# Kernel optimization log

Hardware: AMD Instinct MI355X
Metric: run time of the kernel (lower is better)

## Reference

```python
import jax, jax.numpy as jnp
import numpy as np


def setup_inputs() -> dict:
    key = jax.random.key(0)
    k1, k2 = jax.random.split(key)
    B, N, M = 8, 8192, 8192
    input1 = jax.random.normal(k1, (B, N, 3), dtype=jnp.float32)
    input2 = jax.random.normal(k2, (B, M, 3), dtype=jnp.float32)
    return {"input1": input1, "input2": input2}


def _chamfer(xyz1, xyz2):
    # xyz1: [B, N, 3], xyz2: [B, M, 3]
    sq1 = jnp.sum(xyz1 * xyz1, axis=-1)              # [B, N]
    sq2 = jnp.sum(xyz2 * xyz2, axis=-1)              # [B, M]
    cross = jnp.einsum("bnd,bmd->bnm", xyz1, xyz2)  # [B, N, M]
    d = sq1[:, :, None] + sq2[:, None, :] - 2.0 * cross
    dist1 = jnp.min(d, axis=2)  # [B, N] nearest in xyz2 for each pt of xyz1
    dist2 = jnp.min(d, axis=1)  # [B, M]
    return dist1, dist2


def reference(input1, input2):
    return _chamfer(input1, input2)
```

## Files before the change

kernel.cpp:

```cpp
#include <hip/hip_runtime.h>


typedef __attribute__((ext_vector_type(8))) short  s16x8;
typedef __attribute__((ext_vector_type(16))) float f32x16;
typedef unsigned int u32;

#define TSLICE 512
#define QPB    512
#define QPW    128

__device__ inline u32 umin3(u32 a, u32 b, u32 c) {
    const u32 t = a < b ? a : b;
    return t < c ? t : c;
}

__device__ inline void mfma_fold_phys(const s16x8 a, const s16x8 b, u32& best) {
    asm volatile(
        "v_mfma_f32_32x32x16_bf16 v[40:55], %1, %2, 0\n\t"
        "s_nop 7\n\t"
        "s_nop 7\n\t"
        "s_nop 7\n\t"
        "v_min3_u32 v56, v40, v41, v42\n\t"
        "v_min3_u32 v57, v43, v44, v45\n\t"
        "v_min3_u32 v58, v46, v47, v48\n\t"
        "v_min3_u32 v59, v49, v50, v51\n\t"
        "v_min3_u32 v60, v52, v53, v54\n\t"
        "v_min3_u32 v56, v56, v57, v55\n\t"
        "v_min3_u32 v58, v58, v59, v60\n\t"
        "v_min3_u32 %0, v56, v58, %0"
        : "+v"(best)
        : "v"(a), "v"(b)
        : "v40","v41","v42","v43","v44","v45","v46","v47",
          "v48","v49","v50","v51","v52","v53","v54","v55",
          "v56","v57","v58","v59","v60");
}

__device__ inline unsigned int bf16bits(float v, float &hival) {
    unsigned int u = __float_as_uint(v);
    unsigned int r = (u + 0x7FFFu + ((u >> 16) & 1u)) >> 16;
    hival = __uint_as_float(r << 16);
    return r;
}

__global__ __launch_bounds__(256)
void pack_all_kernel(const float* __restrict__ in1, const float* __restrict__ in2,
                     ushort* __restrict__ A1, ushort* __restrict__ B1, float* __restrict__ S1,
                     ushort* __restrict__ A2, ushort* __restrict__ B2, float* __restrict__ S2,
                     unsigned int* __restrict__ out, int P1, int P2) {
    const int g = blockIdx.x * 256 + threadIdx.x;
    if (g >= P1 + P2) return;
    out[g] = 0x7F7F7F7Fu;

    const float* src; ushort* pA; ushort* pB; float* sq; int p;
    if (g < P1) { src = in1; pA = A1; pB = B1; sq = S1; p = g; }
    else        { src = in2; pA = A2; pB = B2; sq = S2; p = g - P1; }

    const float x = src[3*p+0], y = src[3*p+1], z = src[3*p+2];
    float xhf, xlf, yhf, ylf, zhf, zlf, shf, tmp;
    const ushort xh = (ushort)bf16bits(x, xhf);
    const ushort xl = (ushort)bf16bits(x - xhf, xlf);
    const ushort yh = (ushort)bf16bits(y, yhf);
    const ushort yl = (ushort)bf16bits(y - yhf, ylf);
    const ushort zh = (ushort)bf16bits(z, zhf);
    const ushort zl = (ushort)bf16bits(z - zhf, zlf);
    const float s = fmaf(x, x, fmaf(y, y, z * z));
    const ushort sh = (ushort)bf16bits(s, shf);
    const ushort sl = (ushort)bf16bits(s - shf, tmp);
    const ushort m2xh = (ushort)bf16bits(-2.0f * xhf, tmp);
    const ushort m2xl = (ushort)bf16bits(-2.0f * xlf, tmp);
    const ushort m2yh = (ushort)bf16bits(-2.0f * yhf, tmp);
    const ushort m2yl = (ushort)bf16bits(-2.0f * ylf, tmp);
    const ushort m2zh = (ushort)bf16bits(-2.0f * zhf, tmp);
    const ushort m2zl = (ushort)bf16bits(-2.0f * zlf, tmp);
    const ushort ONE  = 0x3F80;
    const ushort BIAS = 0x4400;

    const s16x8 a0 = {(short)m2xh,(short)m2xl,(short)m2xh,(short)m2xl,
                      (short)m2yh,(short)m2yl,(short)m2yh,(short)m2yl};
    const s16x8 a1 = {(short)m2zh,(short)m2zl,(short)m2zh,(short)m2zl,
                      (short)sh,  (short)sl,  (short)BIAS, 0};
    const s16x8 b0 = {(short)xh,(short)xh,(short)xl,(short)xl,
                      (short)yh,(short)yh,(short)yl,(short)yl};
    const s16x8 b1 = {(short)zh,(short)zh,(short)zl,(short)zl,
                      (short)ONE,(short)ONE,(short)ONE, 0};

    s16x8* A8 = (s16x8*)pA;
    s16x8* B8 = (s16x8*)pB;
    const int c0 = (p & ~31) * 2 + (p & 31);
    A8[c0]      = a0;
    A8[c0 + 32] = a1;
    B8[2*p]     = b0;
    B8[2*p + 1] = b1;
    sq[p] = s;
}

__global__ __launch_bounds__(256)
void chamfer_mfma_kernel(const ushort* __restrict__ Ad1, const ushort* __restrict__ Bd1,
                         const float*  __restrict__ Sd1, unsigned int* __restrict__ Od1,
                         const ushort* __restrict__ Ad2, const ushort* __restrict__ Bd2,
                         const float*  __restrict__ Sd2, unsigned int* __restrict__ Od2,
                         int Np, int Mp) {
    __shared__ s16x8 lds8[TSLICE * 2];
    const int z = blockIdx.z;
    const ushort* pA  = z ? Ad2 : Ad1;
    const ushort* pB  = z ? Bd2 : Bd1;
    const float*  sqq = z ? Sd2 : Sd1;
    unsigned int* out = z ? Od2 : Od1;

    const int tid  = threadIdx.x;
    const int lane = tid & 63;
    const int wid  = tid >> 6;
    const int qblock = blockIdx.x * QPB;
    const int b = qblock / Np;
    const size_t gchunk = ((size_t)b * Mp + (size_t)blockIdx.y * TSLICE) * 2;
    const s16x8* gA = (const s16x8*)pA + gchunk;
    for (int i = tid; i < TSLICE * 2; i += 256) lds8[i] = gA[i];

    const int qw = qblock + wid * QPW;
    s16x8 bfr0, bfr1, bfr2, bfr3;
    {
        const int qb = qw + (lane & 31);
        const size_t hi = (size_t)(lane >> 5) * 8;
        bfr0 = *(const s16x8*)(pB + (size_t)(qb +  0) * 16 + hi);
        bfr1 = *(const s16x8*)(pB + (size_t)(qb + 32) * 16 + hi);
        bfr2 = *(const s16x8*)(pB + (size_t)(qb + 64) * 16 + hi);
        bfr3 = *(const s16x8*)(pB + (size_t)(qb + 96) * 16 + hi);
    }
    __syncthreads();

    u32 b0 = 0x7F7F7F7Fu, b1 = 0x7F7F7F7Fu, b2 = 0x7F7F7F7Fu, b3 = 0x7F7F7F7Fu;

    const int NT = TSLICE / 32;
    s16x8 a = lds8[lane];
    for (int t = 0; t < NT; ++t) {
        const int tn = (t + 1 < NT) ? (t + 1) : t;
        const s16x8 an = lds8[tn * 64 + lane];
        mfma_fold_phys(a, bfr0, b0);
        mfma_fold_phys(a, bfr1, b1);
        mfma_fold_phys(a, bfr2, b2);
        mfma_fold_phys(a, bfr3, b3);
        a = an;
    }

    u32 bests[4] = {b0, b1, b2, b3};
    #pragma unroll
    for (int f = 0; f < 4; ++f) {
        u32 bu = bests[f];
        const u32 other = __shfl_xor(bu, 32);
        bu = bu < other ? bu : other;
        const int q = qw + f * 32 + (lane & 31);
        float v = (__uint_as_float(bu) - 512.0f) + sqq[q];
        v = fmaxf(v, 0.0f);
        if (lane < 32) atomicMin(out + q, __float_as_uint(v));
    }
}

#define FSLICE 512
#define FROWS  512
__global__ __launch_bounds__(256)
void chamfer_dir_kernel(const float* __restrict__ P, const float* __restrict__ Q,
                        unsigned int* __restrict__ out, int Np, int Mp) {
    __shared__ float4 lds[FSLICE];
    const int tid = threadIdx.x;
    const int rowBase = blockIdx.x * FROWS;
    const int b = rowBase / Np;
    const int slice0 = blockIdx.y * FSLICE;
    const float* qs = Q + ((size_t)b * Mp + slice0) * 3;
    #pragma unroll
    for (int i = tid; i < FSLICE; i += 256) {
        const float x = qs[3*i+0], y = qs[3*i+1], z = qs[3*i+2];
        lds[i] = make_float4(x, y, z, fmaf(x, x, fmaf(y, y, z * z)));
    }
    const int q0 = rowBase + tid, q1 = q0 + 256;
    const float* p0 = P + (size_t)q0 * 3;
    const float* p1 = P + (size_t)q1 * 3;
    const float x0=p0[0], y0=p0[1], z0=p0[2], x1=p1[0], y1=p1[1], z1=p1[2];
    const float m2x0=-2*x0, m2y0=-2*y0, m2z0=-2*z0, m2x1=-2*x1, m2y1=-2*y1, m2z1=-2*z1;
    const float sqp0 = fmaf(x0,x0,fmaf(y0,y0,z0*z0));
    const float sqp1 = fmaf(x1,x1,fmaf(y1,y1,z1*z1));
    __syncthreads();
    float best0 = 3.0e38f, best1 = 3.0e38f;
    #pragma unroll 4
    for (int j = 0; j < FSLICE; j += 2) {
        const float4 a = lds[j], c = lds[j+1];
        const float d00 = fmaf(m2x0,a.x,fmaf(m2y0,a.y,fmaf(m2z0,a.z,a.w)));
        const float d01 = fmaf(m2x0,c.x,fmaf(m2y0,c.y,fmaf(m2z0,c.z,c.w)));
        best0 = fminf(fminf(d00,d01), best0);
        const float d10 = fmaf(m2x1,a.x,fmaf(m2y1,a.y,fmaf(m2z1,a.z,a.w)));
        const float d11 = fmaf(m2x1,c.x,fmaf(m2y1,c.y,fmaf(m2z1,c.z,c.w)));
        best1 = fminf(fminf(d10,d11), best1);
    }
    atomicMin(out + q0, __float_as_uint(fmaxf(best0 + sqp0, 0.f)));
    atomicMin(out + q1, __float_as_uint(fmaxf(best1 + sqp1, 0.f)));
}

extern "C" void kernel_launch(void* const* d_in, const int* in_sizes, int n_in,
                              void* d_out, int out_size, void* d_ws, size_t ws_size,
                              hipStream_t stream) {
    const float* in1 = (const float*)d_in[0];
    const float* in2 = (const float*)d_in[1];
    const int B = 8;
    const int N = in_sizes[0] / (B * 3);
    const int M = in_sizes[1] / (B * 3);
    const int P1 = B * N, P2 = B * M;
    unsigned int* out = (unsigned int*)d_out;

    const size_t packBytes1 = (size_t)P1 * 32, packBytes2 = (size_t)P2 * 32;
    const size_t need = 2*packBytes1 + 2*packBytes2 + (size_t)(P1+P2)*4;

    if (ws_size >= need && N == M) {
        char* w = (char*)d_ws;
        ushort* A1 = (ushort*)(w);
        ushort* B1 = (ushort*)(w + packBytes1);
        ushort* A2 = (ushort*)(w + 2*packBytes1);
        ushort* B2 = (ushort*)(w + 2*packBytes1 + packBytes2);
        float*  S1 = (float*) (w + 2*packBytes1 + 2*packBytes2);
        float*  S2 = (float*) (w + 2*packBytes1 + 2*packBytes2 + (size_t)P1*4);

        pack_all_kernel<<<(P1 + P2 + 255)/256, 256, 0, stream>>>(
            in1, in2, A1, B1, S1, A2, B2, S2, out, P1, P2);

        dim3 g(P1 / QPB, M / TSLICE, 2);
        chamfer_mfma_kernel<<<g, 256, 0, stream>>>(
            A2, B1, S1, out,
            A1, B2, S2, out + P1,
            N, M);
    } else {
        hipMemsetAsync(d_out, 0x7F, (size_t)out_size * sizeof(float), stream);
        dim3 g1(P1 / FROWS, M / FSLICE);
        chamfer_dir_kernel<<<g1, 256, 0, stream>>>(in1, in2, out, N, M);
        dim3 g2(P2 / FROWS, N / FSLICE);
        chamfer_dir_kernel<<<g2, 256, 0, stream>>>(in2, in1, out + P1, M, N);
    }
}
```

Measured before the change: 46.59 us.

## Software-pipeline MFMA and min-fold across four accumulator register banks

Replaces the serialized MFMA-then-nop-then-fold asm with a rotating scheme: each step first folds the previous MFMA result held in a dedicated 16-register bank, then issues the next MFMA into that bank. This drops the 24 cycles of s_nop per MFMA and lets the other three banks' MFMAs cover the latency, with a single drain and fold after the loop. Banks are preset to the sentinel so the first fold does nothing. It relies on hard-coded physical VGPRs v48-v116 held live across asm statements without compiler awareness, so correctness depends on the compiler not reusing those registers between the statements.

```diff
diff --git a/kernel.cpp b/kernel.cpp
--- a/kernel.cpp
+++ b/kernel.cpp
@@ -14,26 +14,51 @@
     return t < c ? t : c;
 }
 
-__device__ inline void mfma_fold_phys(const s16x8 a, const s16x8 b, u32& best) {
-    asm volatile(
-        "v_mfma_f32_32x32x16_bf16 v[40:55], %1, %2, 0\n\t"
-        "s_nop 7\n\t"
-        "s_nop 7\n\t"
-        "s_nop 7\n\t"
-        "v_min3_u32 v56, v40, v41, v42\n\t"
-        "v_min3_u32 v57, v43, v44, v45\n\t"
-        "v_min3_u32 v58, v46, v47, v48\n\t"
-        "v_min3_u32 v59, v49, v50, v51\n\t"
-        "v_min3_u32 v60, v52, v53, v54\n\t"
-        "v_min3_u32 v56, v56, v57, v55\n\t"
-        "v_min3_u32 v58, v58, v59, v60\n\t"
-        "v_min3_u32 %0, v56, v58, %0"
-        : "+v"(best)
-        : "v"(a), "v"(b)
-        : "v40","v41","v42","v43","v44","v45","v46","v47",
-          "v48","v49","v50","v51","v52","v53","v54","v55",
-          "v56","v57","v58","v59","v60");
-}
+#define STEP_ASM(B0,B1,B2,B3,B4,B5,B6,B7,B8,B9,B10,B11,B12,B13,B14,B15,RANGE) \
+    asm volatile( \
+        "v_min3_u32 v112, v" #B0 ", v" #B1 ", v" #B2 "\n\t" \
+        "v_min3_u32 v113, v" #B3 ", v" #B4 ", v" #B5 "\n\t" \
+        "v_min3_u32 v114, v" #B6 ", v" #B7 ", v" #B8 "\n\t" \
+        "v_min3_u32 v115, v" #B9 ", v" #B10 ", v" #B11 "\n\t" \
+        "v_min3_u32 v116, v" #B12 ", v" #B13 ", v" #B14 "\n\t" \
+        "v_min3_u32 v112, v112, v113, v" #B15 "\n\t" \
+        "v_min3_u32 v114, v114, v115, v116\n\t" \
+        "v_min3_u32 %0, v112, v114, %0\n\t" \
+        "v_mfma_f32_32x32x16_bf16 " RANGE ", %1, %2, 0" \
+        : "+v"(best) : "v"(a), "v"(b) \
+        : "v" #B0, "v" #B1, "v" #B2, "v" #B3, "v" #B4, "v" #B5, "v" #B6, \
+          "v" #B7, "v" #B8, "v" #B9, "v" #B10, "v" #B11, "v" #B12, \
+          "v" #B13, "v" #B14, "v" #B15, "v112","v113","v114","v115","v116")
+
+__device__ inline void step_f0(const s16x8 a, const s16x8 b, u32& best) {
+    STEP_ASM(48,49,50,51,52,53,54,55,56,57,58,59,60,61,62,63, "v[48:63]");
+}
+__device__ inline void step_f1(const s16x8 a, const s16x8 b, u32& best) {
+    STEP_ASM(64,65,66,67,68,69,70,71,72,73,74,75,76,77,78,79, "v[64:79]");
+}
+__device__ inline void step_f2(const s16x8 a, const s16x8 b, u32& best) {
+    STEP_ASM(80,81,82,83,84,85,86,87,88,89,90,91,92,93,94,95, "v[80:95]");
+}
+__device__ inline void step_f3(const s16x8 a, const s16x8 b, u32& best) {
+    STEP_ASM(96,97,98,99,100,101,102,103,104,105,106,107,108,109,110,111, "v[96:111]");
+}
+
+#define FOLD_ASM(B0,B1,B2,B3,B4,B5,B6,B7,B8,B9,B10,B11,B12,B13,B14,B15) \
+    asm volatile( \
+        "v_min3_u32 v112, v" #B0 ", v" #B1 ", v" #B2 "\n\t" \
+        "v_min3_u32 v113, v" #B3 ", v" #B4 ", v" #B5 "\n\t" \
+        "v_min3_u32 v114, v" #B6 ", v" #B7 ", v" #B8 "\n\t" \
+        "v_min3_u32 v115, v" #B9 ", v" #B10 ", v" #B11 "\n\t" \
+        "v_min3_u32 v116, v" #B12 ", v" #B13 ", v" #B14 "\n\t" \
+        "v_min3_u32 v112, v112, v113, v" #B15 "\n\t" \
+        "v_min3_u32 v114, v114, v115, v116\n\t" \
+        "v_min3_u32 %0, v112, v114, %0" \
+        : "+v"(best) :: "v112","v113","v114","v115","v116")
+
+__device__ inline void fold_f0(u32& best) { FOLD_ASM(48,49,50,51,52,53,54,55,56,57,58,59,60,61,62,63); }
+__device__ inline void fold_f1(u32& best) { FOLD_ASM(64,65,66,67,68,69,70,71,72,73,74,75,76,77,78,79); }
+__device__ inline void fold_f2(u32& best) { FOLD_ASM(80,81,82,83,84,85,86,87,88,89,90,91,92,93,94,95); }
+__device__ inline void fold_f3(u32& best) { FOLD_ASM(96,97,98,99,100,101,102,103,104,105,106,107,108,109,110,111); }
 
 __device__ inline unsigned int bf16bits(float v, float &hival) {
     unsigned int u = __float_as_uint(v);
@@ -128,6 +153,48 @@
     }
     __syncthreads();
 
+    asm volatile(
+        "v_mov_b32 v48, 0x7f7f7f7f\n\tv_mov_b32 v49, 0x7f7f7f7f\n\t"
+        "v_mov_b32 v50, 0x7f7f7f7f\n\tv_mov_b32 v51, 0x7f7f7f7f\n\t"
+        "v_mov_b32 v52, 0x7f7f7f7f\n\tv_mov_b32 v53, 0x7f7f7f7f\n\t"
+        "v_mov_b32 v54, 0x7f7f7f7f\n\tv_mov_b32 v55, 0x7f7f7f7f\n\t"
+        "v_mov_b32 v56, 0x7f7f7f7f\n\tv_mov_b32 v57, 0x7f7f7f7f\n\t"
+        "v_mov_b32 v58, 0x7f7f7f7f\n\tv_mov_b32 v59, 0x7f7f7f7f\n\t"
+        "v_mov_b32 v60, 0x7f7f7f7f\n\tv_mov_b32 v61, 0x7f7f7f7f\n\t"
+        "v_mov_b32 v62, 0x7f7f7f7f\n\tv_mov_b32 v63, 0x7f7f7f7f\n\t"
+        "v_mov_b32 v64, 0x7f7f7f7f\n\tv_mov_b32 v65, 0x7f7f7f7f\n\t"
+        "v_mov_b32 v66, 0x7f7f7f7f\n\tv_mov_b32 v67, 0x7f7f7f7f\n\t"
+        "v_mov_b32 v68, 0x7f7f7f7f\n\tv_mov_b32 v69, 0x7f7f7f7f\n\t"
+        "v_mov_b32 v70, 0x7f7f7f7f\n\tv_mov_b32 v71, 0x7f7f7f7f\n\t"
+        "v_mov_b32 v72, 0x7f7f7f7f\n\tv_mov_b32 v73, 0x7f7f7f7f\n\t"
+        "v_mov_b32 v74, 0x7f7f7f7f\n\tv_mov_b32 v75, 0x7f7f7f7f\n\t"
+        "v_mov_b32 v76, 0x7f7f7f7f\n\tv_mov_b32 v77, 0x7f7f7f7f\n\t"
+        "v_mov_b32 v78, 0x7f7f7f7f\n\tv_mov_b32 v79, 0x7f7f7f7f\n\t"
+        "v_mov_b32 v80, 0x7f7f7f7f\n\tv_mov_b32 v81, 0x7f7f7f7f\n\t"
+        "v_mov_b32 v82, 0x7f7f7f7f\n\tv_mov_b32 v83, 0x7f7f7f7f\n\t"
+        "v_mov_b32 v84, 0x7f7f7f7f\n\tv_mov_b32 v85, 0x7f7f7f7f\n\t"
+        "v_mov_b32 v86, 0x7f7f7f7f\n\tv_mov_b32 v87, 0x7f7f7f7f\n\t"
+        "v_mov_b32 v88, 0x7f7f7f7f\n\tv_mov_b32 v89, 0x7f7f7f7f\n\t"
+        "v_mov_b32 v90, 0x7f7f7f7f\n\tv_mov_b32 v91, 0x7f7f7f7f\n\t"
+        "v_mov_b32 v92, 0x7f7f7f7f\n\tv_mov_b32 v93, 0x7f7f7f7f\n\t"
+        "v_mov_b32 v94, 0x7f7f7f7f\n\tv_mov_b32 v95, 0x7f7f7f7f\n\t"
+        "v_mov_b32 v96, 0x7f7f7f7f\n\tv_mov_b32 v97, 0x7f7f7f7f\n\t"
+        "v_mov_b32 v98, 0x7f7f7f7f\n\tv_mov_b32 v99, 0x7f7f7f7f\n\t"
+        "v_mov_b32 v100, 0x7f7f7f7f\n\tv_mov_b32 v101, 0x7f7f7f7f\n\t"
+        "v_mov_b32 v102, 0x7f7f7f7f\n\tv_mov_b32 v103, 0x7f7f7f7f\n\t"
+        "v_mov_b32 v104, 0x7f7f7f7f\n\tv_mov_b32 v105, 0x7f7f7f7f\n\t"
+        "v_mov_b32 v106, 0x7f7f7f7f\n\tv_mov_b32 v107, 0x7f7f7f7f\n\t"
+        "v_mov_b32 v108, 0x7f7f7f7f\n\tv_mov_b32 v109, 0x7f7f7f7f\n\t"
+        "v_mov_b32 v110, 0x7f7f7f7f\n\tv_mov_b32 v111, 0x7f7f7f7f"
+        ::: "v48","v49","v50","v51","v52","v53","v54","v55",
+            "v56","v57","v58","v59","v60","v61","v62","v63",
+            "v64","v65","v66","v67","v68","v69","v70","v71",
+            "v72","v73","v74","v75","v76","v77","v78","v79",
+            "v80","v81","v82","v83","v84","v85","v86","v87",
+            "v88","v89","v90","v91","v92","v93","v94","v95",
+            "v96","v97","v98","v99","v100","v101","v102","v103",
+            "v104","v105","v106","v107","v108","v109","v110","v111");
+
     u32 b0 = 0x7F7F7F7Fu, b1 = 0x7F7F7F7Fu, b2 = 0x7F7F7F7Fu, b3 = 0x7F7F7F7Fu;
 
     const int NT = TSLICE / 32;
@@ -135,12 +202,15 @@
     for (int t = 0; t < NT; ++t) {
         const int tn = (t + 1 < NT) ? (t + 1) : t;
         const s16x8 an = lds8[tn * 64 + lane];
-        mfma_fold_phys(a, bfr0, b0);
-        mfma_fold_phys(a, bfr1, b1);
-        mfma_fold_phys(a, bfr2, b2);
-        mfma_fold_phys(a, bfr3, b3);
+        step_f0(a, bfr0, b0);
+        step_f1(a, bfr1, b1);
+        step_f2(a, bfr2, b2);
+        step_f3(a, bfr3, b3);
         a = an;
     }
+
+    asm volatile("s_nop 7\n\ts_nop 7\n\ts_nop 7");
+    fold_f0(b0); fold_f1(b1); fold_f2(b2); fold_f3(b3);
 
     u32 bests[4] = {b0, b1, b2, b3};
     #pragma unroll
```

Result: no change. 46.33 us (-0.5%).
